# Kernel optimization log

Hardware: AMD Instinct MI355X
Metric: run time of the kernel (lower is better)

Reference implementation:

```python
import jax, jax.numpy as jnp
import numpy as np

WS = 8          # window_size
HEAD_DIM = 32
N_HEADS = 6     # input_dim // head_dim = 192 // 32
SHIFT = WS // 2 # cyclic shift for 'SW' type


def _rel_index():
    # per (query, key) pair inside a window: relative coord index into (2*WS-1, 2*WS-1) table
    cord = np.array([[i, j] for i in range(WS) for j in range(WS)])  # [p*p, 2]
    rel = cord[:, None, :] - cord[None, :, :] + WS - 1               # [pp, pp, 2]
    return rel[:, :, 0], rel[:, :, 1]


def _shift_mask(hw, ww):
    # boolean additive mask for shifted windows (True -> -inf), flattened to [nw, pp, pp]
    p, s = WS, WS - SHIFT
    m = np.zeros((hw, ww, p, p, p, p), dtype=bool)
    m[-1, :, :s, :, s:, :] = True
    m[-1, :, s:, :, :s, :] = True
    m[:, -1, :, :s, :, s:] = True
    m[:, -1, :, s:, :, :s] = True
    return jnp.asarray(m.reshape(hw * ww, p * p, p * p))


def setup_inputs() -> dict:
    key = jax.random.key(0)
    ks = jax.random.split(key, 6)
    C = N_HEADS * HEAD_DIM  # 192
    x = jax.random.normal(ks[0], (4, 256, 256, C), jnp.float32)
    w_qkv = jax.random.normal(ks[1], (C, 3 * C), jnp.float32) * 0.02
    b_qkv = jnp.zeros((3 * C,), jnp.float32)
    rel_pos = jax.random.normal(ks[2], (N_HEADS, 2 * WS - 1, 2 * WS - 1), jnp.float32) * 0.02
    w_out = jax.random.normal(ks[3], (C, C), jnp.float32) * 0.02
    b_out = jnp.zeros((C,), jnp.float32)
    return dict(x=x, w_qkv=w_qkv, b_qkv=b_qkv, rel_pos=rel_pos, w_out=w_out, b_out=b_out)


def reference(x, w_qkv, b_qkv, rel_pos, w_out, b_out):
    B, H, W, C = x.shape
    scale = HEAD_DIM ** -0.5
    # SW type: cyclic shift (H,W divisible by WS so no padding needed)
    x = jnp.roll(x, (-SHIFT, -SHIFT), axis=(1, 2))
    hw, ww = H // WS, W // WS
    nw, pp = hw * ww, WS * WS
    # window partition: [B, nw, pp, C]
    xw = x.reshape(B, hw, WS, ww, WS, C).transpose(0, 1, 3, 2, 4, 5).reshape(B, nw, pp, C)
    qkv = xw @ w_qkv + b_qkv                                   # [B, nw, pp, 3C]
    qkv = qkv.reshape(B, nw, pp, 3 * N_HEADS, HEAD_DIM)
    qkv = jnp.moveaxis(qkv, 3, 0)                              # [3h, B, nw, pp, c]
    q, k, v = qkv[:N_HEADS], qkv[N_HEADS:2 * N_HEADS], qkv[2 * N_HEADS:]
    sim = jnp.einsum('hbwpc,hbwqc->hbwpq', q, k) * scale       # [h, B, nw, pp, pp]
    r0, r1 = _rel_index()
    sim = sim + rel_pos[:, r0, r1][:, None, None]              # relative position bias
    mask = _shift_mask(hw, ww)                                 # [nw, pp, pp]
    sim = jnp.where(mask[None, None], -jnp.inf, sim)
    probs = jax.nn.softmax(sim, axis=-1)
    out = jnp.einsum('hbwpq,hbwqc->hbwpc', probs, v)           # [h, B, nw, pp, c]
    out = jnp.moveaxis(out, 0, 3).reshape(B, nw, pp, C)        # merge heads
    out = out @ w_out + b_out
    # window merge back to [B, H, W, C]
    out = out.reshape(B, hw, ww, WS, WS, C).transpose(0, 1, 3, 2, 4, 5).reshape(B, H, W, C)
    out = jnp.roll(out, (SHIFT, SHIFT), axis=(1, 2))
    return out
```

## Files before the change

kernel.cpp:

```cpp
#include <hip/hip_runtime.h>
#include <stdint.h>


typedef __bf16 bf16x8 __attribute__((ext_vector_type(8)));
typedef float f32x16 __attribute__((ext_vector_type(16)));
typedef unsigned int uint2v __attribute__((ext_vector_type(2)));

#define MFMA32 __builtin_amdgcn_mfma_f32_32x32x16_bf16

#define WOUT_OFF 110592
#define BIAS_OFF 147456
#define SIM_SCALE 0.1767766952966369f

static __device__ __forceinline__ unsigned short f2bf(float f) {
  return __builtin_bit_cast(unsigned short, (__bf16)f);
}
static __device__ __forceinline__ float bf2f(unsigned short u) {
  unsigned int x = ((unsigned int)u) << 16;
  return __builtin_bit_cast(float, x);
}
static __device__ __forceinline__ unsigned int pk2(float a, float b) {
  return (unsigned int)f2bf(a) | ((unsigned int)f2bf(b) << 16);
}
static __device__ __forceinline__ bf16x8 mk8(unsigned int a, unsigned int b,
                                             unsigned int c, unsigned int d) {
  uint4 t; t.x = a; t.y = b; t.z = c; t.w = d;
  return __builtin_bit_cast(bf16x8, t);
}

__global__ void pack_kernel(const float* __restrict__ wqkv,
                            const float* __restrict__ wout,
                            const float* __restrict__ relpos,
                            unsigned short* __restrict__ ws) {
  int tid = blockIdx.x * 256 + threadIdx.x;
  if (tid < 13824) {
    int lane = tid & 63, t = tid >> 6;
    int ks = t / 18, nt = t - ks * 18;
    int n = nt * 32 + (lane & 31);
    int c0 = ks * 16 + (lane >> 5) * 8;
    unsigned short v[8];
#pragma unroll
    for (int j = 0; j < 8; ++j) v[j] = f2bf(wqkv[(size_t)(c0 + j) * 576 + n]);
    ushort4 a; a.x = v[0]; a.y = v[1]; a.z = v[2]; a.w = v[3];
    ushort4 bq; bq.x = v[4]; bq.y = v[5]; bq.z = v[6]; bq.w = v[7];
    *(ushort4*)(ws + (size_t)tid * 8) = a;
    *(ushort4*)(ws + (size_t)tid * 8 + 4) = bq;
  } else if (tid < 13824 + 4608) {
    int id = tid - 13824;
    int lane = id & 63, t = id >> 6;
    int ks = t / 6, oct = t - ks * 6;
    int oc = oct * 32 + (lane & 31);
    int c0 = ks * 16 + (lane >> 5) * 8;
    unsigned short v[8];
#pragma unroll
    for (int j = 0; j < 8; ++j) v[j] = f2bf(wout[(size_t)(c0 + j) * 192 + oc]);
    ushort4 a; a.x = v[0]; a.y = v[1]; a.z = v[2]; a.w = v[3];
    ushort4 bq; bq.x = v[4]; bq.y = v[5]; bq.z = v[6]; bq.w = v[7];
    *(ushort4*)(ws + WOUT_OFF + (size_t)id * 8) = a;
    *(ushort4*)(ws + WOUT_OFF + (size_t)id * 8 + 4) = bq;
  } else if (tid < 13824 + 4608 + 384) {
    int id = tid - 18432;
    int h = id >> 6, p = id & 63;
    int pr = p >> 3, pc = p & 7;
#pragma unroll
    for (int q4 = 0; q4 < 16; ++q4) {
      unsigned short v[4];
#pragma unroll
      for (int j = 0; j < 4; ++j) {
        int q = q4 * 4 + j;
        int r0 = pr - (q >> 3) + 7;
        int r1 = pc - (q & 7) + 7;
        v[j] = f2bf(relpos[h * 225 + r0 * 15 + r1]);
      }
      ushort4 o; o.x = v[0]; o.y = v[1]; o.z = v[2]; o.w = v[3];
      *(ushort4*)(ws + BIAS_OFF + (size_t)(h * 64 + p) * 64 + q4 * 4) = o;
    }
  }
}

__global__ __launch_bounds__(256, 2)
void wmsa_kernel(const float* __restrict__ x, const float* __restrict__ bqkv,
                 const float* __restrict__ bout, const unsigned short* __restrict__ ws,
                 float* __restrict__ out) {
  __shared__ __align__(16) unsigned char smem[73728];

  const int tidx = threadIdx.x;
  const int wid = tidx >> 6, lane = tidx & 63;
  const int lo5 = lane & 31, hi = lane >> 5;
  const int bid = blockIdx.x;
  const int b = bid >> 10, widx = bid & 1023;
  const int wh = widx >> 5, ww = widx & 31;

  const int mt = wid & 1;
  const int ntbase = (wid >> 1) * 9;

  const int m = mt * 32 + lo5;
  const int gh0 = (wh * 8 + (m >> 3) + 4) & 255;
  const int gw0 = (ww * 8 + (m & 7) + 4) & 255;
  const float* xtok = x + ((size_t)((b * 256 + gh0) * 256 + gw0)) * 192;

  const uint4* wqkvP = (const uint4*)ws;
  const uint4* woutP = (const uint4*)(ws + WOUT_OFF);
  const unsigned short* biasT = ws + BIAS_OFF;

  f32x16 acc[9] = {};
#pragma unroll
  for (int ks = 0; ks < 12; ++ks) {
    const float4 xa = *(const float4*)(xtok + ks * 16 + hi * 8);
    const float4 xb = *(const float4*)(xtok + ks * 16 + hi * 8 + 4);
    const bf16x8 xf = mk8(pk2(xa.x, xa.y), pk2(xa.z, xa.w),
                          pk2(xb.x, xb.y), pk2(xb.z, xb.w));
#pragma unroll
    for (int t = 0; t < 9; ++t) {
      const uint4 w = wqkvP[(size_t)((ks * 18 + ntbase + t) * 64 + lane)];
      acc[t] = MFMA32(__builtin_bit_cast(bf16x8, w), xf, acc[t], 0, 0, 0);
    }
  }

#pragma unroll
  for (int t = 0; t < 9; ++t) {
    const int nt = ntbase + t;
    if (nt < 12) {
      unsigned char* base = smem + (nt < 6 ? 0 : 24576);
      const int col0 = (nt < 6 ? nt : nt - 6) * 32;
#pragma unroll
      for (int g = 0; g < 4; ++g) {
        const float4 bq = *(const float4*)(bqkv + nt * 32 + 8 * g + 4 * hi);
        const float bqa[4] = {bq.x, bq.y, bq.z, bq.w};
        const int c0 = col0 + 8 * g + 4 * hi;
        ushort4 wv;
        wv.x = f2bf(acc[t][4 * g + 0] + bqa[0]);
        wv.y = f2bf(acc[t][4 * g + 1] + bqa[1]);
        wv.z = f2bf(acc[t][4 * g + 2] + bqa[2]);
        wv.w = f2bf(acc[t][4 * g + 3] + bqa[3]);
        *(ushort4*)(base + m * 384 + ((c0 * 2) ^ ((m & 7) << 4))) = wv;
      }
    } else {
      const int h = nt - 12;
#pragma unroll
      for (int g = 0; g < 4; ++g) {
        const float4 bq = *(const float4*)(bqkv + nt * 32 + 8 * g + 4 * hi);
        const float bqa[4] = {bq.x, bq.y, bq.z, bq.w};
#pragma unroll
        for (int j = 0; j < 4; ++j) {
          const int d = 8 * g + 4 * hi + j;
          *(unsigned short*)(smem + 49152 + h * 4096 + d * 128 +
                             ((m * 2) ^ ((d & 7) << 4))) =
              f2bf(acc[t][4 * g + j] + bqa[j]);
        }
      }
    }
  }
  __syncthreads();

  const bool lastRow = (wh == 31), lastCol = (ww == 31);
  f32x16 oacc[3];
  float oscale[3];
#pragma unroll
  for (int u = 0; u < 3; ++u) {
    const int idx = wid * 3 + u;
    const int h = idx >> 1, ph = idx & 1;
    const int p = ph * 32 + lo5;
    const int swz = (lo5 & 7) << 4;

    const bf16x8 qf0 = *(const bf16x8*)(smem + p * 384 + ((h * 64 + 0 + hi * 16) ^ swz));
    const bf16x8 qf1 = *(const bf16x8*)(smem + p * 384 + ((h * 64 + 32 + hi * 16) ^ swz));

    f32x16 s0 = {}, s1 = {};
    {
      bf16x8 kf;
      kf = *(const bf16x8*)(smem + 24576 + lo5 * 384 + ((h * 64 + 0 + hi * 16) ^ swz));
      s0 = MFMA32(kf, qf0, s0, 0, 0, 0);
      kf = *(const bf16x8*)(smem + 24576 + lo5 * 384 + ((h * 64 + 32 + hi * 16) ^ swz));
      s0 = MFMA32(kf, qf1, s0, 0, 0, 0);
      kf = *(const bf16x8*)(smem + 24576 + (32 + lo5) * 384 + ((h * 64 + 0 + hi * 16) ^ swz));
      s1 = MFMA32(kf, qf0, s1, 0, 0, 0);
      kf = *(const bf16x8*)(smem + 24576 + (32 + lo5) * 384 + ((h * 64 + 32 + hi * 16) ^ swz));
      s1 = MFMA32(kf, qf1, s1, 0, 0, 0);
    }

    float pv[2][16];
    const bool pA = (p >> 3) < 4;
    const bool mcol = lastCol && (((p & 7) < 4) != (hi == 0));
#pragma unroll
    for (int rt = 0; rt < 2; ++rt) {
      const bool mk = (lastRow && (pA != (rt == 0))) || mcol;
#pragma unroll
      for (int g = 0; g < 4; ++g) {
        const ushort4 bb = *(const ushort4*)(biasT + (size_t)(h * 64 + p) * 64 +
                                             rt * 32 + 8 * g + 4 * hi);
        const unsigned short bbv[4] = {bb.x, bb.y, bb.z, bb.w};
#pragma unroll
        for (int j = 0; j < 4; ++j) {
          const int r = 4 * g + j;
          const float v = (rt == 0 ? s0[r] : s1[r]) * SIM_SCALE + bf2f(bbv[j]);
          pv[rt][r] = mk ? -1e30f : v;
        }
      }
    }

    float mx = pv[0][0];
#pragma unroll
    for (int r = 1; r < 16; ++r) mx = fmaxf(mx, pv[0][r]);
#pragma unroll
    for (int r = 0; r < 16; ++r) mx = fmaxf(mx, pv[1][r]);
    mx = fmaxf(mx, __shfl_xor(mx, 32));
    float sum = 0.f;
#pragma unroll
    for (int rt = 0; rt < 2; ++rt)
#pragma unroll
      for (int r = 0; r < 16; ++r) {
        const float e = __expf(pv[rt][r] - mx);
        pv[rt][r] = e;
        sum += e;
      }
    sum += __shfl_xor(sum, 32);
    oscale[u] = __builtin_amdgcn_rcpf(sum);

    f32x16 oa = {};
#pragma unroll
    for (int rt = 0; rt < 2; ++rt) {
      const unsigned int W0 = pk2(pv[rt][0], pv[rt][1]);
      const unsigned int W1 = pk2(pv[rt][2], pv[rt][3]);
      const unsigned int W2 = pk2(pv[rt][4], pv[rt][5]);
      const unsigned int W3 = pk2(pv[rt][6], pv[rt][7]);
      const unsigned int W4 = pk2(pv[rt][8], pv[rt][9]);
      const unsigned int W5 = pk2(pv[rt][10], pv[rt][11]);
      const unsigned int W6 = pk2(pv[rt][12], pv[rt][13]);
      const unsigned int W7 = pk2(pv[rt][14], pv[rt][15]);
      const uint2v r0 = __builtin_amdgcn_permlane32_swap(W0, W2, false, false);
      const uint2v r1 = __builtin_amdgcn_permlane32_swap(W1, W3, false, false);
      const uint2v r2 = __builtin_amdgcn_permlane32_swap(W4, W6, false, false);
      const uint2v r3 = __builtin_amdgcn_permlane32_swap(W5, W7, false, false);
      const bf16x8 f0 = mk8(r0[0], r1[0], r0[1], r1[1]);
      const bf16x8 f1 = mk8(r2[0], r3[0], r2[1], r3[1]);
      const bf16x8 va = *(const bf16x8*)(smem + 49152 + h * 4096 + lo5 * 128 +
                                         (((rt * 2 + 0) * 32 + hi * 16) ^ swz));
      oa = MFMA32(va, f0, oa, 0, 0, 0);
      const bf16x8 vb = *(const bf16x8*)(smem + 49152 + h * 4096 + lo5 * 128 +
                                         (((rt * 2 + 1) * 32 + hi * 16) ^ swz));
      oa = MFMA32(vb, f1, oa, 0, 0, 0);
    }
    oacc[u] = oa;
  }
  __syncthreads();

#pragma unroll
  for (int u = 0; u < 3; ++u) {
    const int idx = wid * 3 + u;
    const int h = idx >> 1, ph = idx & 1;
    const int p = ph * 32 + lo5;
    const float sc = oscale[u];
#pragma unroll
    for (int g = 0; g < 4; ++g) {
      ushort4 wv;
      wv.x = f2bf(oacc[u][4 * g + 0] * sc);
      wv.y = f2bf(oacc[u][4 * g + 1] * sc);
      wv.z = f2bf(oacc[u][4 * g + 2] * sc);
      wv.w = f2bf(oacc[u][4 * g + 3] * sc);
      const int c0 = h * 32 + 8 * g + 4 * hi;
      *(ushort4*)(smem + p * 384 + ((c0 * 2) ^ ((p & 7) << 4))) = wv;
    }
  }
  __syncthreads();

  const int octb = (wid >> 1) * 3;
  f32x16 po[3] = {};
#pragma unroll
  for (int ks = 0; ks < 12; ++ks) {
    const bf16x8 af = *(const bf16x8*)(smem + (mt * 32 + lo5) * 384 +
                                       ((ks * 32 + hi * 16) ^ ((lo5 & 7) << 4)));
#pragma unroll
    for (int j = 0; j < 3; ++j) {
      const uint4 w = woutP[(size_t)((ks * 6 + octb + j) * 64 + lane)];
      po[j] = MFMA32(af, __builtin_bit_cast(bf16x8, w), po[j], 0, 0, 0);
    }
  }
#pragma unroll
  for (int j = 0; j < 3; ++j) {
    const int oc = (octb + j) * 32 + lo5;
    const float bo = bout[oc];
#pragma unroll
    for (int r = 0; r < 16; ++r) {
      const int tok = mt * 32 + (r & 3) + 8 * (r >> 2) + 4 * hi;
      const int gh = (wh * 8 + (tok >> 3) + 4) & 255;
      const int gw = (ww * 8 + (tok & 7) + 4) & 255;
      out[(size_t)((b * 256 + gh) * 256 + gw) * 192 + oc] = po[j][r] + bo;
    }
  }
}

extern "C" void kernel_launch(void* const* d_in, const int* in_sizes, int n_in,
                              void* d_out, int out_size, void* d_ws, size_t ws_size,
                              hipStream_t stream) {
  const float* x = (const float*)d_in[0];
  const float* wqkv = (const float*)d_in[1];
  const float* bqkv = (const float*)d_in[2];
  const float* relpos = (const float*)d_in[3];
  const float* wout = (const float*)d_in[4];
  const float* bout = (const float*)d_in[5];
  float* out = (float*)d_out;
  unsigned short* ws = (unsigned short*)d_ws;

  pack_kernel<<<dim3(74), dim3(256), 0, stream>>>(wqkv, wout, relpos, ws);
  wmsa_kernel<<<dim3(4096), dim3(256), 0, stream>>>(x, bqkv, bout, ws, out);
}
```

Measured before the change: 504.9 us.

## Shrink shared memory to 48KB by time-multiplexing Q/K/V buffers for 3 blocks/CU

Reassigns QKV output tiles so each wave-group owns Q or K columns plus a slice of V heads. V stays in registers until the QK/softmax phase completes and then overwrites the Q/K region. The attention output tile is then written to the freed K area. This cuts LDS from 72KB to 48KB and raises launch bounds to 3 blocks per CU for more occupancy, at the cost of an extra barrier and higher register pressure from holding V accumulators and packed probabilities across phases.

```diff
diff --git a/kernel.cpp b/kernel.cpp
--- a/kernel.cpp
+++ b/kernel.cpp
@@ -78,11 +78,11 @@
   }
 }
 
-__global__ __launch_bounds__(256, 2)
+__global__ __launch_bounds__(256, 3)
 void wmsa_kernel(const float* __restrict__ x, const float* __restrict__ bqkv,
                  const float* __restrict__ bout, const unsigned short* __restrict__ ws,
                  float* __restrict__ out) {
-  __shared__ __align__(16) unsigned char smem[73728];
+  __shared__ __align__(16) unsigned char smem[49152];
 
   const int tidx = threadIdx.x;
   const int wid = tidx >> 6, lane = tidx & 63;
@@ -91,8 +91,8 @@
   const int b = bid >> 10, widx = bid & 1023;
   const int wh = widx >> 5, ww = widx & 31;
 
+  const int grp = wid >> 1;
   const int mt = wid & 1;
-  const int ntbase = (wid >> 1) * 9;
 
   const int m = mt * 32 + lo5;
   const int gh0 = (wh * 8 + (m >> 3) + 4) & 255;
@@ -112,17 +112,18 @@
                           pk2(xb.x, xb.y), pk2(xb.z, xb.w));
 #pragma unroll
     for (int t = 0; t < 9; ++t) {
-      const uint4 w = wqkvP[(size_t)((ks * 18 + ntbase + t) * 64 + lane)];
+      const int nt = (t < 6) ? (grp * 6 + t) : (12 + grp * 3 + (t - 6));
+      const uint4 w = wqkvP[(size_t)((ks * 18 + nt) * 64 + lane)];
       acc[t] = MFMA32(__builtin_bit_cast(bf16x8, w), xf, acc[t], 0, 0, 0);
     }
   }
 
-#pragma unroll
-  for (int t = 0; t < 9; ++t) {
-    const int nt = ntbase + t;
-    if (nt < 12) {
-      unsigned char* base = smem + (nt < 6 ? 0 : 24576);
-      const int col0 = (nt < 6 ? nt : nt - 6) * 32;
+  {
+    unsigned char* base = smem + grp * 24576;
+#pragma unroll
+    for (int t = 0; t < 6; ++t) {
+      const int nt = grp * 6 + t;
+      const int col0 = t * 32;
 #pragma unroll
       for (int g = 0; g < 4; ++g) {
         const float4 bq = *(const float4*)(bqkv + nt * 32 + 8 * g + 4 * hi);
@@ -135,26 +136,12 @@
         wv.w = f2bf(acc[t][4 * g + 3] + bqa[3]);
         *(ushort4*)(base + m * 384 + ((c0 * 2) ^ ((m & 7) << 4))) = wv;
       }
-    } else {
-      const int h = nt - 12;
-#pragma unroll
-      for (int g = 0; g < 4; ++g) {
-        const float4 bq = *(const float4*)(bqkv + nt * 32 + 8 * g + 4 * hi);
-        const float bqa[4] = {bq.x, bq.y, bq.z, bq.w};
-#pragma unroll
-        for (int j = 0; j < 4; ++j) {
-          const int d = 8 * g + 4 * hi + j;
-          *(unsigned short*)(smem + 49152 + h * 4096 + d * 128 +
-                             ((m * 2) ^ ((d & 7) << 4))) =
-              f2bf(acc[t][4 * g + j] + bqa[j]);
-        }
-      }
     }
   }
   __syncthreads();
 
   const bool lastRow = (wh == 31), lastCol = (ww == 31);
-  f32x16 oacc[3];
+  bf16x8 pf[3][4];
   float oscale[3];
 #pragma unroll
   for (int u = 0; u < 3; ++u) {
@@ -217,7 +204,6 @@
     sum += __shfl_xor(sum, 32);
     oscale[u] = __builtin_amdgcn_rcpf(sum);
 
-    f32x16 oa = {};
 #pragma unroll
     for (int rt = 0; rt < 2; ++rt) {
       const unsigned int W0 = pk2(pv[rt][0], pv[rt][1]);
@@ -232,18 +218,48 @@
       const uint2v r1 = __builtin_amdgcn_permlane32_swap(W1, W3, false, false);
       const uint2v r2 = __builtin_amdgcn_permlane32_swap(W4, W6, false, false);
       const uint2v r3 = __builtin_amdgcn_permlane32_swap(W5, W7, false, false);
-      const bf16x8 f0 = mk8(r0[0], r1[0], r0[1], r1[1]);
-      const bf16x8 f1 = mk8(r2[0], r3[0], r2[1], r3[1]);
-      const bf16x8 va = *(const bf16x8*)(smem + 49152 + h * 4096 + lo5 * 128 +
+      pf[u][rt * 2 + 0] = mk8(r0[0], r1[0], r0[1], r1[1]);
+      pf[u][rt * 2 + 1] = mk8(r2[0], r3[0], r2[1], r3[1]);
+    }
+  }
+  __syncthreads();
+
+#pragma unroll
+  for (int t = 6; t < 9; ++t) {
+    const int h = grp * 3 + (t - 6);
+    const int nt = 12 + h;
+#pragma unroll
+    for (int g = 0; g < 4; ++g) {
+      const float4 bq = *(const float4*)(bqkv + nt * 32 + 8 * g + 4 * hi);
+      const float bqa[4] = {bq.x, bq.y, bq.z, bq.w};
+#pragma unroll
+      for (int j = 0; j < 4; ++j) {
+        const int d = 8 * g + 4 * hi + j;
+        *(unsigned short*)(smem + h * 4096 + d * 128 + ((m * 2) ^ ((d & 7) << 4))) =
+            f2bf(acc[t][4 * g + j] + bqa[j]);
+      }
+    }
+  }
+  __syncthreads();
+
+  f32x16 oacc[3];
+#pragma unroll
+  for (int u = 0; u < 3; ++u) {
+    const int idx = wid * 3 + u;
+    const int h = idx >> 1;
+    const int swz = (lo5 & 7) << 4;
+    f32x16 oa = {};
+#pragma unroll
+    for (int rt = 0; rt < 2; ++rt) {
+      const bf16x8 va = *(const bf16x8*)(smem + h * 4096 + lo5 * 128 +
                                          (((rt * 2 + 0) * 32 + hi * 16) ^ swz));
-      oa = MFMA32(va, f0, oa, 0, 0, 0);
-      const bf16x8 vb = *(const bf16x8*)(smem + 49152 + h * 4096 + lo5 * 128 +
+      oa = MFMA32(va, pf[u][rt * 2 + 0], oa, 0, 0, 0);
+      const bf16x8 vb = *(const bf16x8*)(smem + h * 4096 + lo5 * 128 +
                                          (((rt * 2 + 1) * 32 + hi * 16) ^ swz));
-      oa = MFMA32(vb, f1, oa, 0, 0, 0);
+      oa = MFMA32(vb, pf[u][rt * 2 + 1], oa, 0, 0, 0);
     }
     oacc[u] = oa;
   }
-  __syncthreads();
 
 #pragma unroll
   for (int u = 0; u < 3; ++u) {
@@ -259,16 +275,16 @@
       wv.z = f2bf(oacc[u][4 * g + 2] * sc);
       wv.w = f2bf(oacc[u][4 * g + 3] * sc);
       const int c0 = h * 32 + 8 * g + 4 * hi;
-      *(ushort4*)(smem + p * 384 + ((c0 * 2) ^ ((p & 7) << 4))) = wv;
+      *(ushort4*)(smem + 24576 + p * 384 + ((c0 * 2) ^ ((p & 7) << 4))) = wv;
     }
   }
   __syncthreads();
 
-  const int octb = (wid >> 1) * 3;
+  const int octb = grp * 3;
   f32x16 po[3] = {};
 #pragma unroll
   for (int ks = 0; ks < 12; ++ks) {
-    const bf16x8 af = *(const bf16x8*)(smem + (mt * 32 + lo5) * 384 +
+    const bf16x8 af = *(const bf16x8*)(smem + 24576 + (mt * 32 + lo5) * 384 +
                                        ((ks * 32 + hi * 16) ^ ((lo5 & 7) << 4)));
 #pragma unroll
     for (int j = 0; j < 3; ++j) {
```

After: 1.115 ms. 2.21x slower.
